# Performance work log

Hardware: AMD Instinct MI355X
Metric: run time of the kernel (lower is better)

The kernel has to match this reference:

```python
import jax, jax.numpy as jnp
import numpy as np

B, N, F_IN, DIM, TOPK = 64, 1024, 10, 64, 20
EPS = 1e-5  # BatchNorm eps
NEG_SLOPE = 0.2


def _bn_eval(x, gamma, beta, mean, var):
    # eval-mode BatchNorm1d over the channel (last) axis
    return (x - mean) * jax.lax.rsqrt(var + EPS) * gamma + beta


def setup_inputs() -> dict:
    key = jax.random.key(0)
    ks = jax.random.split(key, 10)
    return {
        "data": jax.random.normal(ks[0], (B, N, F_IN), jnp.float32),
        "emb": jax.random.normal(ks[1], (N, DIM), jnp.float32),
        "W_lin": jax.random.normal(ks[2], (F_IN, DIM), jnp.float32),
        "att_i": jax.random.normal(ks[3], (DIM,), jnp.float32),
        "att_j": jax.random.normal(ks[4], (DIM,), jnp.float32),
        "att_em_i": jax.random.normal(ks[5], (DIM,), jnp.float32),
        "att_em_j": jax.random.normal(ks[6], (DIM,), jnp.float32),
        "gnn_bias": jax.random.normal(ks[7], (DIM,), jnp.float32),
        "bn1_gamma": jnp.ones((DIM,), jnp.float32),
        "bn1_beta": jnp.zeros((DIM,), jnp.float32),
        "bn1_mean": jnp.zeros((DIM,), jnp.float32),
        "bn1_var": jnp.ones((DIM,), jnp.float32),
        "bn2_gamma": jnp.ones((DIM,), jnp.float32),
        "bn2_beta": jnp.zeros((DIM,), jnp.float32),
        "bn2_mean": jnp.zeros((DIM,), jnp.float32),
        "bn2_var": jnp.ones((DIM,), jnp.float32),
        "out_W": jax.random.normal(ks[8], (DIM, 1), jnp.float32),
        "out_b": jax.random.normal(ks[9], (1,), jnp.float32),
    }


def reference(data, emb, W_lin, att_i, att_j, att_em_i, att_em_j, gnn_bias,
              bn1_gamma, bn1_beta, bn1_mean, bn1_var,
              bn2_gamma, bn2_beta, bn2_mean, bn2_var, out_W, out_b):
    Bn, Nn, _ = data.shape
    BN_nodes = Bn * Nn
    x = data.reshape(BN_nodes, -1)                      # [B*N, F_IN] (input is detached in torch)

    # ---- dynamic graph: cosine similarity of (detached) node embeddings, top-k per row ----
    w = jax.lax.stop_gradient(emb)                      # weights_arr = embedding.detach()
    norms = jnp.linalg.norm(w, axis=-1)                 # [N]
    cos = (w @ w.T) / (norms[:, None] * norms[None, :])  # [N, N]
    topk_idx = jax.lax.top_k(cos, TOPK)[1]              # [N, K], gated_j (message sources)
    src = topk_idx.reshape(-1)                          # j
    dst = jnp.repeat(jnp.arange(Nn), TOPK)              # i
    offs = (jnp.arange(Bn) * Nn)[:, None]               # per-graph node offsets
    bsrc = (src[None, :] + offs).reshape(-1)            # [B*N*K]
    bdst = (dst[None, :] + offs).reshape(-1)
    self_mask = bsrc == bdst                            # edges killed by remove_self_loops
    loops = jnp.arange(BN_nodes)                        # add_self_loops
    e_src = jnp.concatenate([bsrc, loops])              # [E]
    e_dst = jnp.concatenate([bdst, loops])
    e_mask = jnp.concatenate([self_mask, jnp.zeros(BN_nodes, bool)])

    # ---- GAT-style attention message passing (heads=1, concat=False, aggr='add') ----
    h = x @ W_lin                                       # [B*N, DIM]
    h_i, h_j = h[e_dst], h[e_src]                       # gathers, [E, DIM]
    emb_i = emb[e_dst % Nn]                             # embedding repeated per batch graph
    emb_j = emb[e_src % Nn]
    logit = (h_i * att_i).sum(-1) + (emb_i * att_em_i).sum(-1) \
          + (h_j * att_j).sum(-1) + (emb_j * att_em_j).sum(-1)  # [E]
    logit = jnp.where(logit > 0, logit, NEG_SLOPE * logit)       # leaky_relu(0.2)
    logit = jnp.where(e_mask, -1e30, logit)             # removed self-loops get zero weight
    seg_max = jax.ops.segment_max(logit, e_dst, num_segments=BN_nodes)
    ex = jnp.where(e_mask, 0.0, jnp.exp(logit - seg_max[e_dst]))
    seg_sum = jax.ops.segment_sum(ex, e_dst, num_segments=BN_nodes)
    alpha = ex / seg_sum[e_dst]                         # segment softmax over incoming edges
    agg = jax.ops.segment_sum(h_j * alpha[:, None], e_dst, num_segments=BN_nodes)
    agg = agg + gnn_bias                                # [B*N, DIM]
    gcn = jax.nn.relu(_bn_eval(agg, bn1_gamma, bn1_beta, bn1_mean, bn1_var))

    # ---- output head: multiply by node embedding, BN+ReLU, Linear(DIM->1) ----
    y = gcn.reshape(Bn, Nn, DIM) * emb[None, :, :]
    y = jax.nn.relu(_bn_eval(y, bn2_gamma, bn2_beta, bn2_mean, bn2_var))
    out = y @ out_W + out_b                             # [B, N, 1]; dropout is inference no-op
    return out.reshape(Bn, Nn)
```

## Files before the change

kernel.cpp:

```cpp
#include <hip/hip_runtime.h>

#define N_NODES 1024
#define B_SZ 64
#define F_IN 10
#define DIM 64
#define TOPK 20
#define BN_TOT (B_SZ * N_NODES)

#define GEMM_BLKS 256
#define PREP_BLKS 256
#define HSCAL_BLKS 4096

__global__ __launch_bounds__(256) void k_build(
    const float* __restrict__ data, const float* __restrict__ emb,
    const float* __restrict__ W_lin,
    const float* __restrict__ att_i, const float* __restrict__ att_j,
    const float* __restrict__ att_em_i, const float* __restrict__ att_em_j,
    const float* __restrict__ gnn_bias,
    const float* __restrict__ g1, const float* __restrict__ b1,
    const float* __restrict__ m1, const float* __restrict__ v1,
    const float* __restrict__ g2, const float* __restrict__ b2,
    const float* __restrict__ m2, const float* __restrict__ v2,
    float* __restrict__ g, float* __restrict__ h,
    float* __restrict__ dd, float* __restrict__ ss,
    float* __restrict__ edi, float* __restrict__ esi, float* __restrict__ nrm,
    float4* __restrict__ bnp) {
    const int bid = blockIdx.x;
    const int t = threadIdx.x;
    const int lane = t & 63, w = t >> 6;

    if (bid < GEMM_BLKS) {
        __shared__ float As[64][65];
        __shared__ float Bs[64][65];
        const int r0 = (bid >> 4) * 64, c0 = (bid & 15) * 64;
#pragma unroll
        for (int k = 0; k < 16; ++k) {
            int idx = t + k * 256;
            int rr = idx >> 6, cc = idx & 63;
            As[rr][cc] = emb[(r0 + rr) * DIM + cc];
            Bs[rr][cc] = emb[(c0 + rr) * DIM + cc];
        }
        __syncthreads();
        const int tx = t & 15, ty = t >> 4;
        float acc[4][4] = {};
#pragma unroll 8
        for (int d = 0; d < 64; ++d) {
            float a[4], b[4];
#pragma unroll
            for (int ii = 0; ii < 4; ++ii) a[ii] = As[ty * 4 + ii][d];
#pragma unroll
            for (int jj = 0; jj < 4; ++jj) b[jj] = Bs[tx * 4 + jj][d];
#pragma unroll
            for (int ii = 0; ii < 4; ++ii)
#pragma unroll
                for (int jj = 0; jj < 4; ++jj) acc[ii][jj] += a[ii] * b[jj];
        }
#pragma unroll
        for (int ii = 0; ii < 4; ++ii)
#pragma unroll
            for (int jj = 0; jj < 4; ++jj)
                g[(r0 + ty * 4 + ii) * N_NODES + (c0 + tx * 4 + jj)] = acc[ii][jj];
        return;
    }

    if (bid < GEMM_BLKS + PREP_BLKS) {
        const int node = (bid - GEMM_BLKS) * 4 + w;
        float e = emb[node * DIM + lane];
        float t1 = e * att_em_i[lane];
        float t2 = e * att_em_j[lane];
        float t3 = e * e;
#pragma unroll
        for (int m = 32; m >= 1; m >>= 1) {
            t1 += __shfl_xor(t1, m, 64);
            t2 += __shfl_xor(t2, m, 64);
            t3 += __shfl_xor(t3, m, 64);
        }
        if (lane == 0) { edi[node] = t1; esi[node] = t2; nrm[node] = sqrtf(t3); }
        if (bid == GEMM_BLKS && t < DIM) {
            float a1 = g1[t] * rsqrtf(v1[t] + 1e-5f);
            float c1 = (gnn_bias[t] - m1[t]) * a1 + b1[t];
            float a2 = g2[t] * rsqrtf(v2[t] + 1e-5f);
            float c2 = b2[t] - m2[t] * a2;
            bnp[t] = make_float4(a1, c1, a2, c2);
        }
        return;
    }

    {
        const int base = (bid - GEMM_BLKS - PREP_BLKS) * 16 + w * 4;
        float wl[F_IN];
#pragma unroll
        for (int f = 0; f < F_IN; ++f) wl[f] = W_lin[f * DIM + lane];
        const float ai = att_i[lane], aj = att_j[lane];
#pragma unroll
        for (int r = 0; r < 4; ++r) {
            const int node = base + r;
            const float* dp = data + node * F_IN;
            float hv = 0.f;
#pragma unroll
            for (int f = 0; f < F_IN; ++f) hv = fmaf(dp[f], wl[f], hv);
            h[node * DIM + lane] = hv;
            float s1 = hv * ai;
            float s2 = hv * aj;
#pragma unroll
            for (int m = 32; m >= 1; m >>= 1) {
                s1 += __shfl_xor(s1, m, 64);
                s2 += __shfl_xor(s2, m, 64);
            }
            if (lane == 0) { dd[node] = s1; ss[node] = s2; }
        }
    }
}

__global__ __launch_bounds__(256) void k_topk(const float* __restrict__ g,
                                              const float* __restrict__ nrm,
                                              int* __restrict__ tk) {
    __shared__ float cv[4][20];
    __shared__ int ci[4][20];
    const int i = blockIdx.x;
    const int t = threadIdx.x;
    const int lane = t & 63, w = t >> 6;
    const float ni = nrm[i];
    float4 gv = ((const float4*)(g + (size_t)i * N_NODES))[t];
    float4 nv = ((const float4*)nrm)[t];
    float v[4];
    v[0] = gv.x / (ni * nv.x);
    v[1] = gv.y / (ni * nv.y);
    v[2] = gv.z / (ni * nv.z);
    v[3] = gv.w / (ni * nv.w);
    for (int it = 0; it < TOPK; ++it) {
        float bv = v[0];
        int bq = 0;
#pragma unroll
        for (int q = 1; q < 4; ++q)
            if (v[q] > bv) { bv = v[q]; bq = q; }
        int bidx = t * 4 + bq;
#pragma unroll
        for (int m = 32; m >= 1; m >>= 1) {
            float ov = __shfl_xor(bv, m, 64);
            int oi = __shfl_xor(bidx, m, 64);
            if (ov > bv || (ov == bv && oi < bidx)) { bv = ov; bidx = oi; }
        }
        if (lane == 0) { cv[w][it] = bv; ci[w][it] = bidx; }
        if ((bidx >> 2) == t) v[bidx & 3] = -3.0e38f;
    }
    __syncthreads();
    if (w == 0) {
        float mv[4];
        int mi[4];
#pragma unroll
        for (int q = 0; q < 4; ++q) {
            if (lane < TOPK) { mv[q] = cv[q][lane]; mi[q] = ci[q][lane]; }
            else { mv[q] = -3.0e38f; mi[q] = 0x7fffffff; }
        }
        for (int it = 0; it < TOPK; ++it) {
            float bv = mv[0];
            int bq = 0;
#pragma unroll
            for (int q = 1; q < 4; ++q)
                if (mv[q] > bv || (mv[q] == bv && mi[q] < mi[bq])) { bv = mv[q]; bq = q; }
            int bidx = mi[bq];
#pragma unroll
            for (int m = 32; m >= 1; m >>= 1) {
                float ov = __shfl_xor(bv, m, 64);
                int oi = __shfl_xor(bidx, m, 64);
                if (ov > bv || (ov == bv && oi < bidx)) { bv = ov; bidx = oi; }
            }
            if (lane == 0) tk[i * TOPK + it] = bidx;
#pragma unroll
            for (int q = 0; q < 4; ++q)
                if (mi[q] == bidx) mv[q] = -3.0e38f;
        }
    }
}

__global__ __launch_bounds__(256) void k_main(
    const float* __restrict__ h, const float* __restrict__ emb,
    const float* __restrict__ dd, const float* __restrict__ ss,
    const float* __restrict__ edi, const float* __restrict__ esi,
    const int* __restrict__ tk, const float4* __restrict__ bnp,
    const float* __restrict__ outW, const float* __restrict__ outB,
    float* __restrict__ out) {
    const int bid = blockIdx.x;
    const int nb = (bid & 7) * 2048 + (bid >> 3);
    const int w = threadIdx.x >> 6, lane = threadIdx.x & 63;
    const int node = nb * 4 + w;
    const int i = node & (N_NODES - 1);
    const int bbase = node & ~(N_NODES - 1);

    int j = i;
    if (lane < TOPK) j = tk[i * TOPK + lane];

    float ssv = 0.f, esv = 0.f;
    if (lane <= TOPK) { ssv = ss[bbase + j]; esv = esi[j]; }
    const float dde = dd[node] + edi[i];

    const float* hb = h + (size_t)bbase * DIM + lane;
    float hv[TOPK + 1];
#pragma unroll
    for (int k = 0; k < TOPK; ++k) {
        int jk = __builtin_amdgcn_readlane(j, k);
        hv[k] = hb[(size_t)jk * DIM];
    }
    hv[TOPK] = hb[(size_t)i * DIM];

    const bool masked = (lane < TOPK) && (j == i);
    float lg = -3.0e38f;
    if (lane <= TOPK) {
        float l = dde + ssv + esv;
        l = (l > 0.f) ? l : 0.2f * l;
        lg = masked ? -3.0e38f : l;
    }
    float m = lg;
#pragma unroll
    for (int mm = 16; mm >= 1; mm >>= 1) m = fmaxf(m, __shfl_xor(m, mm, 64));
    float ex = (lane <= TOPK && !masked) ? __expf(lg - m) : 0.f;
    float s = ex;
#pragma unroll
    for (int mm = 16; mm >= 1; mm >>= 1) s += __shfl_xor(s, mm, 64);
    const float alpha = ex / s;

    float agg = 0.f;
#pragma unroll
    for (int k = 0; k <= TOPK; ++k) {
        int ab = __builtin_amdgcn_readlane(__float_as_int(alpha), k);
        agg = fmaf(__int_as_float(ab), hv[k], agg);
    }

    const float4 p = bnp[lane];
    float x1 = fmaxf(fmaf(agg, p.x, p.y), 0.f);
    float y = x1 * emb[i * DIM + lane];
    float x2 = fmaxf(fmaf(y, p.z, p.w), 0.f);
    float o = x2 * outW[lane];
#pragma unroll
    for (int mm = 32; mm >= 1; mm >>= 1) o += __shfl_xor(o, mm, 64);
    if (lane == 0) out[node] = o + outB[0];
}

extern "C" void kernel_launch(void* const* d_in, const int* in_sizes, int n_in,
                              void* d_out, int out_size, void* d_ws, size_t ws_size,
                              hipStream_t stream) {
    const float* data     = (const float*)d_in[0];
    const float* emb      = (const float*)d_in[1];
    const float* W_lin    = (const float*)d_in[2];
    const float* att_i    = (const float*)d_in[3];
    const float* att_j    = (const float*)d_in[4];
    const float* att_em_i = (const float*)d_in[5];
    const float* att_em_j = (const float*)d_in[6];
    const float* gnn_bias = (const float*)d_in[7];
    const float* g1 = (const float*)d_in[8];
    const float* b1 = (const float*)d_in[9];
    const float* m1 = (const float*)d_in[10];
    const float* v1 = (const float*)d_in[11];
    const float* g2 = (const float*)d_in[12];
    const float* b2 = (const float*)d_in[13];
    const float* m2 = (const float*)d_in[14];
    const float* v2 = (const float*)d_in[15];
    const float* outW = (const float*)d_in[16];
    const float* outB = (const float*)d_in[17];
    float* out = (float*)d_out;

    float* ws = (float*)d_ws;
    float* g     = ws;
    float* h     = ws + (1 << 20);
    float* dd    = h + (size_t)BN_TOT * DIM;
    float* ss    = dd + BN_TOT;
    float* edi   = ss + BN_TOT;
    float* esi   = edi + N_NODES;
    float* nrm   = esi + N_NODES;
    int*   tk    = (int*)(nrm + N_NODES);
    float4* bnp  = (float4*)(tk + N_NODES * TOPK);

    k_build<<<GEMM_BLKS + PREP_BLKS + HSCAL_BLKS, 256, 0, stream>>>(
        data, emb, W_lin, att_i, att_j, att_em_i, att_em_j, gnn_bias,
        g1, b1, m1, v1, g2, b2, m2, v2,
        g, h, dd, ss, edi, esi, nrm, bnp);
    k_topk<<<N_NODES, 256, 0, stream>>>(g, nrm, tk);
    k_main<<<BN_TOT / 4, 256, 0, stream>>>(h, emb, dd, ss, edi, esi, tk, bnp,
                                           outW, outB, out);
}
```

Measured before the change: 83.68 us.

## Fuse cosine top-k into build kernel and store node features as bf16

Removes the separate Gram-matrix write and top-k kernel. Each of 256 blocks now computes cosine similarities for four rows directly from LDS tiles of the embedding and selects the top-20 in registers. The embedding attention terms are folded into the per-node dd/ss scalars. The projected features h are stored as bf16, halving the gather traffic in the main kernel. This trades one launch and a 4 MB intermediate for recomputed column norms per block, and bf16 rounding of h may perturb results.

```diff
diff --git a/kernel.cpp b/kernel.cpp
--- a/kernel.cpp
+++ b/kernel.cpp
@@ -1,4 +1,5 @@
 #include <hip/hip_runtime.h>
+#include <hip/hip_bf16.h>
 
 #define N_NODES 1024
 #define B_SZ 64
@@ -7,9 +8,9 @@
 #define TOPK 20
 #define BN_TOT (B_SZ * N_NODES)
 
-#define GEMM_BLKS 256
-#define PREP_BLKS 256
-#define HSCAL_BLKS 4096
+#define GT_BLKS 256
+#define HS_BLKS 4096
+#define AB_BLKS (GT_BLKS + 1 + HS_BLKS)
 
 __global__ __launch_bounds__(256) void k_build(
     const float* __restrict__ data, const float* __restrict__ emb,
@@ -21,62 +22,63 @@
     const float* __restrict__ m1, const float* __restrict__ v1,
     const float* __restrict__ g2, const float* __restrict__ b2,
     const float* __restrict__ m2, const float* __restrict__ v2,
-    float* __restrict__ g, float* __restrict__ h,
-    float* __restrict__ dd, float* __restrict__ ss,
-    float* __restrict__ edi, float* __restrict__ esi, float* __restrict__ nrm,
-    float4* __restrict__ bnp) {
+    __hip_bfloat16* __restrict__ h, float* __restrict__ ddt,
+    float* __restrict__ sst, int* __restrict__ tk, float4* __restrict__ bnp) {
     const int bid = blockIdx.x;
     const int t = threadIdx.x;
     const int lane = t & 63, w = t >> 6;
 
-    if (bid < GEMM_BLKS) {
-        __shared__ float As[64][65];
-        __shared__ float Bs[64][65];
-        const int r0 = (bid >> 4) * 64, c0 = (bid & 15) * 64;
-#pragma unroll
-        for (int k = 0; k < 16; ++k) {
-            int idx = t + k * 256;
-            int rr = idx >> 6, cc = idx & 63;
-            As[rr][cc] = emb[(r0 + rr) * DIM + cc];
-            Bs[rr][cc] = emb[(c0 + rr) * DIM + cc];
-        }
+    if (bid < GT_BLKS) {
+        __shared__ float As[4][64];
+        __shared__ float P[64][65];
+        const int r0 = bid * 4;
+        As[t >> 6][t & 63] = emb[(r0 + (t >> 6)) * DIM + (t & 63)];
         __syncthreads();
-        const int tx = t & 15, ty = t >> 4;
-        float acc[4][4] = {};
-#pragma unroll 8
-        for (int d = 0; d < 64; ++d) {
-            float a[4], b[4];
-#pragma unroll
-            for (int ii = 0; ii < 4; ++ii) a[ii] = As[ty * 4 + ii][d];
-#pragma unroll
-            for (int jj = 0; jj < 4; ++jj) b[jj] = Bs[tx * 4 + jj][d];
-#pragma unroll
-            for (int ii = 0; ii < 4; ++ii)
-#pragma unroll
-                for (int jj = 0; jj < 4; ++jj) acc[ii][jj] += a[ii] * b[jj];
-        }
-#pragma unroll
-        for (int ii = 0; ii < 4; ++ii)
-#pragma unroll
-            for (int jj = 0; jj < 4; ++jj)
-                g[(r0 + ty * 4 + ii) * N_NODES + (c0 + tx * 4 + jj)] = acc[ii][jj];
+        float av = As[w][lane];
+        float nni = av * av;
+#pragma unroll
+        for (int m = 32; m >= 1; m >>= 1) nni += __shfl_xor(nni, m, 64);
+        const float ni = sqrtf(nni);
+        float v[16];
+        for (int p = 0; p < 16; ++p) {
+            __syncthreads();
+#pragma unroll
+            for (int k = 0; k < 16; ++k) {
+                int idx = t + k * 256;
+                P[idx >> 6][idx & 63] = emb[(p * 64 + (idx >> 6)) * DIM + (idx & 63)];
+            }
+            __syncthreads();
+            float dot = 0.f, nsq = 0.f;
+#pragma unroll
+            for (int d = 0; d < 64; ++d) {
+                float pv = P[lane][d];
+                dot = fmaf(As[w][d], pv, dot);
+                nsq = fmaf(pv, pv, nsq);
+            }
+            v[p] = dot / (ni * sqrtf(nsq));
+        }
+        int* tkr = tk + (r0 + w) * TOPK;
+        for (int it = 0; it < TOPK; ++it) {
+            float bv = v[0];
+            int bp = 0;
+#pragma unroll
+            for (int p = 1; p < 16; ++p)
+                if (v[p] > bv) { bv = v[p]; bp = p; }
+            int bidx = lane + bp * 64;
+#pragma unroll
+            for (int m = 32; m >= 1; m >>= 1) {
+                float ov = __shfl_xor(bv, m, 64);
+                int oi = __shfl_xor(bidx, m, 64);
+                if (ov > bv || (ov == bv && oi < bidx)) { bv = ov; bidx = oi; }
+            }
+            if (lane == 0) tkr[it] = bidx;
+            if ((bidx & 63) == lane) v[bidx >> 6] = -3.0e38f;
+        }
         return;
     }
 
-    if (bid < GEMM_BLKS + PREP_BLKS) {
-        const int node = (bid - GEMM_BLKS) * 4 + w;
-        float e = emb[node * DIM + lane];
-        float t1 = e * att_em_i[lane];
-        float t2 = e * att_em_j[lane];
-        float t3 = e * e;
-#pragma unroll
-        for (int m = 32; m >= 1; m >>= 1) {
-            t1 += __shfl_xor(t1, m, 64);
-            t2 += __shfl_xor(t2, m, 64);
-            t3 += __shfl_xor(t3, m, 64);
-        }
-        if (lane == 0) { edi[node] = t1; esi[node] = t2; nrm[node] = sqrtf(t3); }
-        if (bid == GEMM_BLKS && t < DIM) {
+    if (bid == GT_BLKS) {
+        if (t < DIM) {
             float a1 = g1[t] * rsqrtf(v1[t] + 1e-5f);
             float c1 = (gnn_bias[t] - m1[t]) * a1 + b1[t];
             float a2 = g2[t] * rsqrtf(v2[t] + 1e-5f);
@@ -87,97 +89,37 @@
     }
 
     {
-        const int base = (bid - GEMM_BLKS - PREP_BLKS) * 16 + w * 4;
+        const int base = (bid - GT_BLKS - 1) * 16 + w * 4;
         float wl[F_IN];
 #pragma unroll
         for (int f = 0; f < F_IN; ++f) wl[f] = W_lin[f * DIM + lane];
         const float ai = att_i[lane], aj = att_j[lane];
+        const float aei = att_em_i[lane], aej = att_em_j[lane];
 #pragma unroll
         for (int r = 0; r < 4; ++r) {
             const int node = base + r;
+            const int i = node & (N_NODES - 1);
+            const float ev = emb[i * DIM + lane];
             const float* dp = data + node * F_IN;
             float hv = 0.f;
 #pragma unroll
             for (int f = 0; f < F_IN; ++f) hv = fmaf(dp[f], wl[f], hv);
-            h[node * DIM + lane] = hv;
-            float s1 = hv * ai;
-            float s2 = hv * aj;
+            h[node * DIM + lane] = __float2bfloat16(hv);
+            float s1 = fmaf(hv, ai, ev * aei);
+            float s2 = fmaf(hv, aj, ev * aej);
 #pragma unroll
             for (int m = 32; m >= 1; m >>= 1) {
                 s1 += __shfl_xor(s1, m, 64);
                 s2 += __shfl_xor(s2, m, 64);
             }
-            if (lane == 0) { dd[node] = s1; ss[node] = s2; }
+            if (lane == 0) { ddt[node] = s1; sst[node] = s2; }
         }
     }
 }
 
-__global__ __launch_bounds__(256) void k_topk(const float* __restrict__ g,
-                                              const float* __restrict__ nrm,
-                                              int* __restrict__ tk) {
-    __shared__ float cv[4][20];
-    __shared__ int ci[4][20];
-    const int i = blockIdx.x;
-    const int t = threadIdx.x;
-    const int lane = t & 63, w = t >> 6;
-    const float ni = nrm[i];
-    float4 gv = ((const float4*)(g + (size_t)i * N_NODES))[t];
-    float4 nv = ((const float4*)nrm)[t];
-    float v[4];
-    v[0] = gv.x / (ni * nv.x);
-    v[1] = gv.y / (ni * nv.y);
-    v[2] = gv.z / (ni * nv.z);
-    v[3] = gv.w / (ni * nv.w);
-    for (int it = 0; it < TOPK; ++it) {
-        float bv = v[0];
-        int bq = 0;
-#pragma unroll
-        for (int q = 1; q < 4; ++q)
-            if (v[q] > bv) { bv = v[q]; bq = q; }
-        int bidx = t * 4 + bq;
-#pragma unroll
-        for (int m = 32; m >= 1; m >>= 1) {
-            float ov = __shfl_xor(bv, m, 64);
-            int oi = __shfl_xor(bidx, m, 64);
-            if (ov > bv || (ov == bv && oi < bidx)) { bv = ov; bidx = oi; }
-        }
-        if (lane == 0) { cv[w][it] = bv; ci[w][it] = bidx; }
-        if ((bidx >> 2) == t) v[bidx & 3] = -3.0e38f;
-    }
-    __syncthreads();
-    if (w == 0) {
-        float mv[4];
-        int mi[4];
-#pragma unroll
-        for (int q = 0; q < 4; ++q) {
-            if (lane < TOPK) { mv[q] = cv[q][lane]; mi[q] = ci[q][lane]; }
-            else { mv[q] = -3.0e38f; mi[q] = 0x7fffffff; }
-        }
-        for (int it = 0; it < TOPK; ++it) {
-            float bv = mv[0];
-            int bq = 0;
-#pragma unroll
-            for (int q = 1; q < 4; ++q)
-                if (mv[q] > bv || (mv[q] == bv && mi[q] < mi[bq])) { bv = mv[q]; bq = q; }
-            int bidx = mi[bq];
-#pragma unroll
-            for (int m = 32; m >= 1; m >>= 1) {
-                float ov = __shfl_xor(bv, m, 64);
-                int oi = __shfl_xor(bidx, m, 64);
-                if (ov > bv || (ov == bv && oi < bidx)) { bv = ov; bidx = oi; }
-            }
-            if (lane == 0) tk[i * TOPK + it] = bidx;
-#pragma unroll
-            for (int q = 0; q < 4; ++q)
-                if (mi[q] == bidx) mv[q] = -3.0e38f;
-        }
-    }
-}
-
 __global__ __launch_bounds__(256) void k_main(
-    const float* __restrict__ h, const float* __restrict__ emb,
-    const float* __restrict__ dd, const float* __restrict__ ss,
-    const float* __restrict__ edi, const float* __restrict__ esi,
+    const __hip_bfloat16* __restrict__ h, const float* __restrict__ emb,
+    const float* __restrict__ ddt, const float* __restrict__ sst,
     const int* __restrict__ tk, const float4* __restrict__ bnp,
     const float* __restrict__ outW, const float* __restrict__ outB,
     float* __restrict__ out) {
@@ -191,23 +133,23 @@
     int j = i;
     if (lane < TOPK) j = tk[i * TOPK + lane];
 
-    float ssv = 0.f, esv = 0.f;
-    if (lane <= TOPK) { ssv = ss[bbase + j]; esv = esi[j]; }
-    const float dde = dd[node] + edi[i];
-
-    const float* hb = h + (size_t)bbase * DIM + lane;
-    float hv[TOPK + 1];
+    float sv = 0.f;
+    if (lane <= TOPK) sv = sst[bbase + j];
+    const float ddv = ddt[node];
+
+    const __hip_bfloat16* hb = h + (size_t)bbase * DIM + lane;
+    float hvf[TOPK + 1];
 #pragma unroll
     for (int k = 0; k < TOPK; ++k) {
         int jk = __builtin_amdgcn_readlane(j, k);
-        hv[k] = hb[(size_t)jk * DIM];
-    }
-    hv[TOPK] = hb[(size_t)i * DIM];
+        hvf[k] = __bfloat162float(hb[(size_t)jk * DIM]);
+    }
+    hvf[TOPK] = __bfloat162float(hb[(size_t)i * DIM]);
 
     const bool masked = (lane < TOPK) && (j == i);
     float lg = -3.0e38f;
     if (lane <= TOPK) {
-        float l = dde + ssv + esv;
+        float l = ddv + sv;
         l = (l > 0.f) ? l : 0.2f * l;
         lg = masked ? -3.0e38f : l;
     }
@@ -224,7 +166,7 @@
 #pragma unroll
     for (int k = 0; k <= TOPK; ++k) {
         int ab = __builtin_amdgcn_readlane(__float_as_int(alpha), k);
-        agg = fmaf(__int_as_float(ab), hv[k], agg);
+        agg = fmaf(__int_as_float(ab), hvf[k], agg);
     }
 
     const float4 p = bnp[lane];
@@ -260,22 +202,17 @@
     const float* outB = (const float*)d_in[17];
     float* out = (float*)d_out;
 
-    float* ws = (float*)d_ws;
-    float* g     = ws;
-    float* h     = ws + (1 << 20);
-    float* dd    = h + (size_t)BN_TOT * DIM;
-    float* ss    = dd + BN_TOT;
-    float* edi   = ss + BN_TOT;
-    float* esi   = edi + N_NODES;
-    float* nrm   = esi + N_NODES;
-    int*   tk    = (int*)(nrm + N_NODES);
-    float4* bnp  = (float4*)(tk + N_NODES * TOPK);
-
-    k_build<<<GEMM_BLKS + PREP_BLKS + HSCAL_BLKS, 256, 0, stream>>>(
+    char* ws = (char*)d_ws;
+    __hip_bfloat16* h = (__hip_bfloat16*)ws;
+    float* ddt  = (float*)(ws + (size_t)8 * 1024 * 1024);
+    float* sst  = ddt + BN_TOT;
+    int*   tk   = (int*)(sst + BN_TOT);
+    float4* bnp = (float4*)(tk + N_NODES * TOPK);
+
+    k_build<<<AB_BLKS, 256, 0, stream>>>(
         data, emb, W_lin, att_i, att_j, att_em_i, att_em_j, gnn_bias,
         g1, b1, m1, v1, g2, b2, m2, v2,
-        g, h, dd, ss, edi, esi, nrm, bnp);
-    k_topk<<<N_NODES, 256, 0, stream>>>(g, nrm, tk);
-    k_main<<<BN_TOT / 4, 256, 0, stream>>>(h, emb, dd, ss, edi, esi, tk, bnp,
+        h, ddt, sst, tk, bnp);
+    k_main<<<BN_TOT / 4, 256, 0, stream>>>(h, emb, ddt, sst, tk, bnp,
                                            outW, outB, out);
 }
```

New measurement: 68.01 us. 18.7% less time.
